# Performance work log

Measured on AMD Instinct MI355X. Metric: run time of the kernel, lower is better.

The kernel has to match this reference:

```python
import jax, jax.numpy as jnp
import numpy as np

B, N, C, E, K = 2, 1024, 128, 64, 20

def setup_inputs() -> dict:
    key = jax.random.key(0)
    ks = jax.random.split(key, 4)
    x = jax.random.normal(ks[0], (B, N, C), dtype=jnp.float32)
    Wl = jax.random.normal(ks[1], (C, E), dtype=jnp.float32) * 0.05
    Wr = jax.random.normal(ks[2], (C, E), dtype=jnp.float32) * 0.05
    att = jax.random.normal(ks[3], (1, E), dtype=jnp.float32) * 0.1
    bl = jnp.zeros((E,), dtype=jnp.float32)
    br = jnp.zeros((E,), dtype=jnp.float32)
    edge_index = jnp.zeros((2, 1), dtype=jnp.int64)
    batch = jnp.zeros((B * N,), dtype=jnp.int64)
    return {"x": x, "Wl": Wl, "bl": bl, "Wr": Wr, "br": br, "att": att,
            "edge_index": edge_index, "batch": batch}

def reference(x, Wl, bl, Wr, br, att, edge_index, batch):
    # x: [B, N, C]
    b, n, _ = x.shape
    x_l = x @ Wl + bl              # [B, N, E]
    x_r = x @ Wr + br              # [B, N, E]
    # dense pairwise scores: leaky_relu(x_l_i + x_r_j) . att  -> [B, N, N]
    x_cat = jax.nn.leaky_relu(x_l[:, :, None, :] + x_r[:, None, :, :], 0.2)
    alpha = jnp.einsum('bijd,d->bij', x_cat, att[0])
    alpha = jnp.nan_to_num(alpha, nan=0.0, posinf=0.0, neginf=0.0)
    k = min(K, n)
    vals, idx = jax.lax.top_k(alpha, k)            # [B, N, k]
    attention = jax.nn.softmax(vals, axis=-1).reshape(-1)  # [B*N*k]
    # edge index construction (dropout p used only in training; eval = identity)
    offset = (jnp.arange(b) * n)[:, None]                      # [B, 1]
    index_i = jnp.tile(jnp.repeat(jnp.arange(n), k)[None, :], (b, 1)) + offset
    index_j = idx.reshape(b, n * k) + offset
    new_edge_index = jnp.stack([index_i.reshape(-1), index_j.reshape(-1)], axis=0)
    return new_edge_index, attention
```

## Files before the change

kernel.cpp:

```cpp
#include <hip/hip_runtime.h>

#define Bq 2
#define Nq 1024
#define Cq 128
#define Eq 64
#define Kq 20
#define TI 8
#define BN (Bq * Nq)
#define BNK (Bq * Nq * Kq)
#define NEGF (-3.0e38f)

#define DPP_F(x, ctrl) __int_as_float(__builtin_amdgcn_update_dpp( \
    __float_as_int(x), __float_as_int(x), (ctrl), 0xf, 0xf, false))
#define DPP_I(x, ctrl) __builtin_amdgcn_update_dpp((x), (x), (ctrl), 0xf, 0xf, false)
#define RL_F(x, l) __int_as_float(__builtin_amdgcn_readlane(__float_as_int(x), (l)))
#define RL_I(x, l) __builtin_amdgcn_readlane((x), (l))
#define QP_XOR1 0xB1
#define QP_XOR2 0x4E
#define ROR4    0x124
#define ROR8    0x128

__global__ __launch_bounds__(128) void proj_kernel(
    const float* __restrict__ x, const float* __restrict__ Wl,
    const float* __restrict__ bl, const float* __restrict__ Wr,
    const float* __restrict__ br, const float* __restrict__ att,
    float* __restrict__ xl, float* __restrict__ xrP, float* __restrict__ rdot) {
  const int row = blockIdx.x;
  const int t = threadIdx.x;
  const int e = t & 63;
  const bool left = (t < 64);
  __shared__ float xs[Cq];
  xs[t] = x[(size_t)row * Cq + t];
  __syncthreads();
  const float* __restrict__ W = left ? Wl : Wr;
  float acc = 0.f;
#pragma unroll 8
  for (int c = 0; c < Cq; ++c) acc = fmaf(xs[c], W[c * Eq + e], acc);
  acc += left ? bl[e] : br[e];
  if (left) {
    xl[(size_t)row * Eq + e] = acc;
  } else {
    xrP[((size_t)(e >> 2) * BN + row) * 4 + (e & 3)] = acc;
    float s = acc * att[e];
    s += DPP_F(s, QP_XOR1);
    s += DPP_F(s, QP_XOR2);
    s += DPP_F(s, ROR4);
    s += DPP_F(s, ROR8);
    const float sd = (RL_F(s, 0) + RL_F(s, 16)) + (RL_F(s, 32) + RL_F(s, 48));
    if (e == 0) rdot[row] = sd;
  }
}

__global__ __launch_bounds__(1024) void attn_kernel(
    const float* __restrict__ xl, const float* __restrict__ xrP,
    const float* __restrict__ rdot, const float* __restrict__ att,
    float* __restrict__ out) {
  const int gi0  = blockIdx.x * TI;
  const int b    = gi0 >> 10;
  const int tid  = threadIdx.x;
  const int lane = tid & 63;
  const int wave = tid >> 6;

  __shared__ float alpha[TI][Nq];

  {
    const int jt = tid & 511;
    const int r0 = __builtin_amdgcn_readfirstlane(tid >> 9) * 4;
    const float* __restrict__ vb  = xrP + (size_t)(b * Nq + jt) * 4;
    const float* __restrict__ xlw = xl + (size_t)(gi0 + r0) * Eq;

    const float rd0 = 1.5f * rdot[b * Nq + jt];
    const float rd1 = 1.5f * rdot[b * Nq + jt + 512];
    float acc[4][2];
#pragma unroll
    for (int r = 0; r < 4; ++r) { acc[r][0] = rd0; acc[r][1] = rd1; }

    float4 nv0 = *(const float4*)(vb);
    float4 nv1 = *(const float4*)(vb + 512 * 4);
    float4 na0 = *(const float4*)(xlw);
    float4 na1 = *(const float4*)(xlw + Eq);
    float4 na2 = *(const float4*)(xlw + 2 * Eq);
    float4 na3 = *(const float4*)(xlw + 3 * Eq);
    float4 nat = *(const float4*)(att);

#pragma unroll
    for (int ch = 0; ch < 16; ++ch) {
      const float4 v0 = nv0, v1 = nv1;
      const float4 a0 = na0, a1 = na1, a2 = na2, a3 = na3, at = nat;
      if (ch < 15) {
        vb += BN * 4;
        nv0 = *(const float4*)(vb);
        nv1 = *(const float4*)(vb + 512 * 4);
        na0 = *(const float4*)(xlw + (ch + 1) * 4);
        na1 = *(const float4*)(xlw + Eq + (ch + 1) * 4);
        na2 = *(const float4*)(xlw + 2 * Eq + (ch + 1) * 4);
        na3 = *(const float4*)(xlw + 3 * Eq + (ch + 1) * 4);
        nat = *(const float4*)(att + (ch + 1) * 4);
      }
      const float* v0p = (const float*)&v0;
      const float* v1p = (const float*)&v1;
      const float* a0p = (const float*)&a0;
      const float* a1p = (const float*)&a1;
      const float* a2p = (const float*)&a2;
      const float* a3p = (const float*)&a3;
      const float* atp = (const float*)&at;
#pragma unroll
      for (int dd = 0; dd < 4; ++dd) {
        const float a = atp[dd];
        const float x0 = v0p[dd], x1 = v1p[dd];
        acc[0][0] = fmaf(fabsf(a0p[dd] + x0), a, acc[0][0]);
        acc[0][1] = fmaf(fabsf(a0p[dd] + x1), a, acc[0][1]);
        acc[1][0] = fmaf(fabsf(a1p[dd] + x0), a, acc[1][0]);
        acc[1][1] = fmaf(fabsf(a1p[dd] + x1), a, acc[1][1]);
        acc[2][0] = fmaf(fabsf(a2p[dd] + x0), a, acc[2][0]);
        acc[2][1] = fmaf(fabsf(a2p[dd] + x1), a, acc[2][1]);
        acc[3][0] = fmaf(fabsf(a3p[dd] + x0), a, acc[3][0]);
        acc[3][1] = fmaf(fabsf(a3p[dd] + x1), a, acc[3][1]);
      }
    }
#pragma unroll
    for (int r = 0; r < 4; ++r) {
      alpha[r0 + r][jt]       = acc[r][0];
      alpha[r0 + r][jt + 512] = acc[r][1];
    }
  }
  __syncthreads();

  if (wave < TI) {
    float vals[16];
#pragma unroll
    for (int s = 0; s < 16; ++s) vals[s] = alpha[wave][lane + 64 * s];

    float lv = vals[0];
    int   pk = lane;
#pragma unroll
    for (int s = 1; s < 16; ++s)
      if (vals[s] > lv) { lv = vals[s]; pk = (s << 6) | lane; }

    float m0 = 0.f, ssum = 0.f, myv = 0.f;
    int myi = 0;
#pragma unroll 1
    for (int round = 0; round < Kq; ++round) {
      float m = lv;
      m = fmaxf(m, DPP_F(m, QP_XOR1));
      m = fmaxf(m, DPP_F(m, QP_XOR2));
      m = fmaxf(m, DPP_F(m, ROR4));
      m = fmaxf(m, DPP_F(m, ROR8));
      const float bv = fmaxf(fmaxf(RL_F(m, 0), RL_F(m, 16)),
                             fmaxf(RL_F(m, 32), RL_F(m, 48)));
      int key = (lv == bv) ? pk : 0x7FFFFFFF;
      key = min(key, DPP_I(key, QP_XOR1));
      key = min(key, DPP_I(key, QP_XOR2));
      key = min(key, DPP_I(key, ROR4));
      key = min(key, DPP_I(key, ROR8));
      const int jsel = min(min(RL_I(key, 0), RL_I(key, 16)),
                           min(RL_I(key, 32), RL_I(key, 48)));
      if (round == 0) m0 = bv;
      ssum += __expf(0.4f * (bv - m0));
      if (lane == round) { myv = bv; myi = jsel; }
      if (lane == (jsel & 63)) {
        const int sk = jsel >> 6;
#pragma unroll
        for (int s = 0; s < 16; ++s)
          if (s == sk) vals[s] = NEGF;
        lv = vals[0]; pk = lane;
#pragma unroll
        for (int s = 1; s < 16; ++s)
          if (vals[s] > lv) { lv = vals[s]; pk = (s << 6) | lane; }
      }
    }

    if (lane < Kq) {
      const int gi = gi0 + wave;
      const float p = __expf(0.4f * (myv - m0)) / ssum;
      const int base = gi * Kq + lane;
      out[base]            = (float)gi;
      out[BNK + base]      = (float)(b * Nq + myi);
      out[2 * BNK + base]  = p;
    }
  }
}

extern "C" void kernel_launch(void* const* d_in, const int* in_sizes, int n_in,
                              void* d_out, int out_size, void* d_ws, size_t ws_size,
                              hipStream_t stream) {
  const float* x   = (const float*)d_in[0];
  const float* Wl  = (const float*)d_in[1];
  const float* bl  = (const float*)d_in[2];
  const float* Wr  = (const float*)d_in[3];
  const float* br  = (const float*)d_in[4];
  const float* att = (const float*)d_in[5];
  float* out = (float*)d_out;

  float* xl   = (float*)d_ws;
  float* xrP  = xl + (size_t)BN * Eq;
  float* rdot = xrP + (size_t)16 * BN * 4;

  proj_kernel<<<BN, 128, 0, stream>>>(x, Wl, bl, Wr, br, att, xl, xrP, rdot);
  attn_kernel<<<BN / TI, 1024, 0, stream>>>(xl, xrP, rdot, att, out);
}
```

Measured before the change: 39.43 us.

## Split fused attention kernel into separate score and top-k kernels via global buffer

The fused score+top-k kernel is split in two. A score kernel writes the full alpha matrix to a global workspace buffer, and a separate top-k kernel launches 512 blocks of 4 waves each to do the selection. The aim is to use more blocks and more parallelism than the old 256 blocks of 1024 threads, where half the waves sat idle during top-k. In exchange it adds a kernel launch and a round trip of 8 MB of scores through global memory (L2/MALL).

```diff
diff --git a/kernel.cpp b/kernel.cpp
--- a/kernel.cpp
+++ b/kernel.cpp
@@ -5,9 +5,8 @@
 #define Cq 128
 #define Eq 64
 #define Kq 20
-#define TI 8
 #define BN (Bq * Nq)
-#define BNK (Bq * Nq * Kq)
+#define BNK (BN * Kq)
 #define NEGF (-3.0e38f)
 
 #define DPP_F(x, ctrl) __int_as_float(__builtin_amdgcn_update_dpp( \
@@ -51,133 +50,126 @@
   }
 }
 
-__global__ __launch_bounds__(1024) void attn_kernel(
+__global__ __launch_bounds__(512) void score_kernel(
     const float* __restrict__ xl, const float* __restrict__ xrP,
     const float* __restrict__ rdot, const float* __restrict__ att,
-    float* __restrict__ out) {
-  const int gi0  = blockIdx.x * TI;
-  const int b    = gi0 >> 10;
-  const int tid  = threadIdx.x;
-  const int lane = tid & 63;
-  const int wave = tid >> 6;
+    float* __restrict__ alphaG) {
+  const int r0g = blockIdx.x * 4;
+  const int b   = r0g >> 10;
+  const int jt  = threadIdx.x;
+  const float* __restrict__ xlw = xl + (size_t)r0g * Eq;
 
-  __shared__ float alpha[TI][Nq];
+  const float rd0 = 1.5f * rdot[b * Nq + jt];
+  const float rd1 = 1.5f * rdot[b * Nq + jt + 512];
+  float acc[4][2];
+#pragma unroll
+  for (int r = 0; r < 4; ++r) { acc[r][0] = rd0; acc[r][1] = rd1; }
 
-  {
-    const int jt = tid & 511;
-    const int r0 = __builtin_amdgcn_readfirstlane(tid >> 9) * 4;
-    const float* __restrict__ vb  = xrP + (size_t)(b * Nq + jt) * 4;
-    const float* __restrict__ xlw = xl + (size_t)(gi0 + r0) * Eq;
-
-    const float rd0 = 1.5f * rdot[b * Nq + jt];
-    const float rd1 = 1.5f * rdot[b * Nq + jt + 512];
-    float acc[4][2];
-#pragma unroll
-    for (int r = 0; r < 4; ++r) { acc[r][0] = rd0; acc[r][1] = rd1; }
-
-    float4 nv0 = *(const float4*)(vb);
-    float4 nv1 = *(const float4*)(vb + 512 * 4);
-    float4 na0 = *(const float4*)(xlw);
-    float4 na1 = *(const float4*)(xlw + Eq);
-    float4 na2 = *(const float4*)(xlw + 2 * Eq);
-    float4 na3 = *(const float4*)(xlw + 3 * Eq);
-    float4 nat = *(const float4*)(att);
+  const float* __restrict__ vb = xrP + (size_t)(b * Nq + jt) * 4;
+  float4 nv0 = *(const float4*)(vb);
+  float4 nv1 = *(const float4*)(vb + 512 * 4);
+  float4 na0 = *(const float4*)(xlw);
+  float4 na1 = *(const float4*)(xlw + Eq);
+  float4 na2 = *(const float4*)(xlw + 2 * Eq);
+  float4 na3 = *(const float4*)(xlw + 3 * Eq);
+  float4 nat = *(const float4*)(att);
 
 #pragma unroll
-    for (int ch = 0; ch < 16; ++ch) {
-      const float4 v0 = nv0, v1 = nv1;
-      const float4 a0 = na0, a1 = na1, a2 = na2, a3 = na3, at = nat;
-      if (ch < 15) {
-        vb += BN * 4;
-        nv0 = *(const float4*)(vb);
-        nv1 = *(const float4*)(vb + 512 * 4);
-        na0 = *(const float4*)(xlw + (ch + 1) * 4);
-        na1 = *(const float4*)(xlw + Eq + (ch + 1) * 4);
-        na2 = *(const float4*)(xlw + 2 * Eq + (ch + 1) * 4);
-        na3 = *(const float4*)(xlw + 3 * Eq + (ch + 1) * 4);
-        nat = *(const float4*)(att + (ch + 1) * 4);
-      }
-      const float* v0p = (const float*)&v0;
-      const float* v1p = (const float*)&v1;
-      const float* a0p = (const float*)&a0;
-      const float* a1p = (const float*)&a1;
-      const float* a2p = (const float*)&a2;
-      const float* a3p = (const float*)&a3;
-      const float* atp = (const float*)&at;
+  for (int ch = 0; ch < 16; ++ch) {
+    const float4 v0 = nv0, v1 = nv1;
+    const float4 a0 = na0, a1 = na1, a2 = na2, a3 = na3, at = nat;
+    if (ch < 15) {
+      vb += BN * 4;
+      nv0 = *(const float4*)(vb);
+      nv1 = *(const float4*)(vb + 512 * 4);
+      na0 = *(const float4*)(xlw + (ch + 1) * 4);
+      na1 = *(const float4*)(xlw + Eq + (ch + 1) * 4);
+      na2 = *(const float4*)(xlw + 2 * Eq + (ch + 1) * 4);
+      na3 = *(const float4*)(xlw + 3 * Eq + (ch + 1) * 4);
+      nat = *(const float4*)(att + (ch + 1) * 4);
+    }
+    const float* v0p = (const float*)&v0;
+    const float* v1p = (const float*)&v1;
+    const float* a0p = (const float*)&a0;
+    const float* a1p = (const float*)&a1;
+    const float* a2p = (const float*)&a2;
+    const float* a3p = (const float*)&a3;
+    const float* atp = (const float*)&at;
 #pragma unroll
-      for (int dd = 0; dd < 4; ++dd) {
-        const float a = atp[dd];
-        const float x0 = v0p[dd], x1 = v1p[dd];
-        acc[0][0] = fmaf(fabsf(a0p[dd] + x0), a, acc[0][0]);
-        acc[0][1] = fmaf(fabsf(a0p[dd] + x1), a, acc[0][1]);
-        acc[1][0] = fmaf(fabsf(a1p[dd] + x0), a, acc[1][0]);
-        acc[1][1] = fmaf(fabsf(a1p[dd] + x1), a, acc[1][1]);
-        acc[2][0] = fmaf(fabsf(a2p[dd] + x0), a, acc[2][0]);
-        acc[2][1] = fmaf(fabsf(a2p[dd] + x1), a, acc[2][1]);
-        acc[3][0] = fmaf(fabsf(a3p[dd] + x0), a, acc[3][0]);
-        acc[3][1] = fmaf(fabsf(a3p[dd] + x1), a, acc[3][1]);
-      }
-    }
-#pragma unroll
-    for (int r = 0; r < 4; ++r) {
-      alpha[r0 + r][jt]       = acc[r][0];
-      alpha[r0 + r][jt + 512] = acc[r][1];
+    for (int dd = 0; dd < 4; ++dd) {
+      const float a = atp[dd];
+      const float x0 = v0p[dd], x1 = v1p[dd];
+      acc[0][0] = fmaf(fabsf(a0p[dd] + x0), a, acc[0][0]);
+      acc[0][1] = fmaf(fabsf(a0p[dd] + x1), a, acc[0][1]);
+      acc[1][0] = fmaf(fabsf(a1p[dd] + x0), a, acc[1][0]);
+      acc[1][1] = fmaf(fabsf(a1p[dd] + x1), a, acc[1][1]);
+      acc[2][0] = fmaf(fabsf(a2p[dd] + x0), a, acc[2][0]);
+      acc[2][1] = fmaf(fabsf(a2p[dd] + x1), a, acc[2][1]);
+      acc[3][0] = fmaf(fabsf(a3p[dd] + x0), a, acc[3][0]);
+      acc[3][1] = fmaf(fabsf(a3p[dd] + x1), a, acc[3][1]);
     }
   }
-  __syncthreads();
+#pragma unroll
+  for (int r = 0; r < 4; ++r) {
+    alphaG[(size_t)(r0g + r) * Nq + jt]       = acc[r][0];
+    alphaG[(size_t)(r0g + r) * Nq + jt + 512] = acc[r][1];
+  }
+}
 
-  if (wave < TI) {
-    float vals[16];
+__global__ __launch_bounds__(256) void topk_kernel(
+    const float* __restrict__ alphaG, float* __restrict__ out) {
+  const int row  = blockIdx.x * 4 + (threadIdx.x >> 6);
+  const int lane = threadIdx.x & 63;
+  const int b    = row >> 10;
+  float vals[16];
 #pragma unroll
-    for (int s = 0; s < 16; ++s) vals[s] = alpha[wave][lane + 64 * s];
+  for (int s = 0; s < 16; ++s) vals[s] = alphaG[(size_t)row * Nq + lane + 64 * s];
 
-    float lv = vals[0];
-    int   pk = lane;
+  float lv = vals[0];
+  int   pk = lane;
 #pragma unroll
-    for (int s = 1; s < 16; ++s)
-      if (vals[s] > lv) { lv = vals[s]; pk = (s << 6) | lane; }
+  for (int s = 1; s < 16; ++s)
+    if (vals[s] > lv) { lv = vals[s]; pk = (s << 6) | lane; }
 
-    float m0 = 0.f, ssum = 0.f, myv = 0.f;
-    int myi = 0;
+  float m0 = 0.f, ssum = 0.f, myv = 0.f;
+  int myi = 0;
 #pragma unroll 1
-    for (int round = 0; round < Kq; ++round) {
-      float m = lv;
-      m = fmaxf(m, DPP_F(m, QP_XOR1));
-      m = fmaxf(m, DPP_F(m, QP_XOR2));
-      m = fmaxf(m, DPP_F(m, ROR4));
-      m = fmaxf(m, DPP_F(m, ROR8));
-      const float bv = fmaxf(fmaxf(RL_F(m, 0), RL_F(m, 16)),
-                             fmaxf(RL_F(m, 32), RL_F(m, 48)));
-      int key = (lv == bv) ? pk : 0x7FFFFFFF;
-      key = min(key, DPP_I(key, QP_XOR1));
-      key = min(key, DPP_I(key, QP_XOR2));
-      key = min(key, DPP_I(key, ROR4));
-      key = min(key, DPP_I(key, ROR8));
-      const int jsel = min(min(RL_I(key, 0), RL_I(key, 16)),
-                           min(RL_I(key, 32), RL_I(key, 48)));
-      if (round == 0) m0 = bv;
-      ssum += __expf(0.4f * (bv - m0));
-      if (lane == round) { myv = bv; myi = jsel; }
-      if (lane == (jsel & 63)) {
-        const int sk = jsel >> 6;
+  for (int round = 0; round < Kq; ++round) {
+    float m = lv;
+    m = fmaxf(m, DPP_F(m, QP_XOR1));
+    m = fmaxf(m, DPP_F(m, QP_XOR2));
+    m = fmaxf(m, DPP_F(m, ROR4));
+    m = fmaxf(m, DPP_F(m, ROR8));
+    const float bv = fmaxf(fmaxf(RL_F(m, 0), RL_F(m, 16)),
+                           fmaxf(RL_F(m, 32), RL_F(m, 48)));
+    int key = (lv == bv) ? pk : 0x7FFFFFFF;
+    key = min(key, DPP_I(key, QP_XOR1));
+    key = min(key, DPP_I(key, QP_XOR2));
+    key = min(key, DPP_I(key, ROR4));
+    key = min(key, DPP_I(key, ROR8));
+    const int jsel = min(min(RL_I(key, 0), RL_I(key, 16)),
+                         min(RL_I(key, 32), RL_I(key, 48)));
+    if (round == 0) m0 = bv;
+    ssum += __expf(0.4f * (bv - m0));
+    if (lane == round) { myv = bv; myi = jsel; }
+    if (lane == (jsel & 63)) {
+      const int sk = jsel >> 6;
 #pragma unroll
-        for (int s = 0; s < 16; ++s)
-          if (s == sk) vals[s] = NEGF;
-        lv = vals[0]; pk = lane;
+      for (int s = 0; s < 16; ++s)
+        if (s == sk) vals[s] = NEGF;
+      lv = vals[0]; pk = lane;
 #pragma unroll
-        for (int s = 1; s < 16; ++s)
-          if (vals[s] > lv) { lv = vals[s]; pk = (s << 6) | lane; }
-      }
+      for (int s = 1; s < 16; ++s)
+        if (vals[s] > lv) { lv = vals[s]; pk = (s << 6) | lane; }
     }
+  }
 
-    if (lane < Kq) {
-      const int gi = gi0 + wave;
-      const float p = __expf(0.4f * (myv - m0)) / ssum;
-      const int base = gi * Kq + lane;
-      out[base]            = (float)gi;
-      out[BNK + base]      = (float)(b * Nq + myi);
-      out[2 * BNK + base]  = p;
-    }
+  if (lane < Kq) {
+    const float p = __expf(0.4f * (myv - m0)) / ssum;
+    const int base = row * Kq + lane;
+    out[base]            = (float)row;
+    out[BNK + base]      = (float)(b * Nq + myi);
+    out[2 * BNK + base]  = p;
   }
 }
 
@@ -192,10 +184,12 @@
   const float* att = (const float*)d_in[5];
   float* out = (float*)d_out;
 
-  float* xl   = (float*)d_ws;
-  float* xrP  = xl + (size_t)BN * Eq;
-  float* rdot = xrP + (size_t)16 * BN * 4;
+  float* xl     = (float*)d_ws;
+  float* xrP    = xl + (size_t)BN * Eq;
+  float* rdot   = xrP + (size_t)16 * BN * 4;
+  float* alphaG = rdot + (size_t)BN;
 
   proj_kernel<<<BN, 128, 0, stream>>>(x, Wl, bl, Wr, br, att, xl, xrP, rdot);
-  attn_kernel<<<BN / TI, 1024, 0, stream>>>(xl, xrP, rdot, att, out);
+  score_kernel<<<BN / 4, 512, 0, stream>>>(xl, xrP, rdot, att, alphaG);
+  topk_kernel<<<BN / 4, 256, 0, stream>>>(alphaG, out);
 }
```

Measured after the change: 55.44 us. 40.6% more time.
